# Kernel optimization log

Hardware: AMD Instinct MI355X
Metric: run time of the kernel (lower is better)

## Reference

```python
import jax, jax.numpy as jnp
import numpy as np

PARALLISM = 128          # Subarray[0]
O_BITS = 8               # ADC_resolution
SCALE = float(2 ** O_BITS - 1)          # 255.0
MAXCURRENT = 0.02 * PARALLISM           # 2.56 ; a_scale/w_scale == 2**32-1 so guards skip them


def setup_inputs() -> dict:
    key = jax.random.key(0)
    k1, k2, k3 = jax.random.split(key, 3)
    B, K, N = 8192, 4096, 4096
    x = jax.random.normal(k1, (B, K), dtype=jnp.float32) * 0.1
    weight = jax.random.normal(k2, (N, K), dtype=jnp.float32)  # torch Linear layout [out, in]
    bias = jax.random.normal(k3, (N,), dtype=jnp.float32)
    return {"x": x, "weight": weight, "bias": bias, "layer": 1}


def _quantize_partial(x):
    # output_quantize.forward: clamp to +/-maxcurrent, scale to [−scale, scale], round (STE), rescale
    y = jnp.clip(x, -MAXCURRENT, MAXCURRENT)
    y = y / MAXCURRENT * SCALE
    y = y + jax.lax.stop_gradient(jnp.round(y) - y)  # Round.apply with straight-through grad
    return y / SCALE * MAXCURRENT


def reference(x, weight, bias, layer):
    # Hard_fc: chunked VMM along the input-feature (row) dim with per-subarray ADC quantization
    B, K = x.shape
    w = weight.T                      # [K, N]
    N = w.shape[1]
    num = K // PARALLISM              # K chosen divisible by PARALLISM (32 chunks)
    xc = x.reshape(B, num, PARALLISM).swapaxes(0, 1)       # [num, B, P]
    wc = w.reshape(num, PARALLISM, N)                       # [num, P, N]

    def step(acc, chunk):
        xi, wi = chunk                # [B, P], [P, N]
        return acc + _quantize_partial(xi @ wi), None

    acc0 = jnp.zeros((B, N), dtype=x.dtype)
    out, _ = jax.lax.scan(step, acc0, (xc, wc))
    out = out + bias
    return out.reshape(B, -1)
```

## Files before the change

### kernel.cpp

```cpp
#include <hip/hip_runtime.h>


typedef __attribute__((ext_vector_type(8))) short short8;
typedef __attribute__((ext_vector_type(4))) float floatx4;

#define BM 128
#define BN 128
#define BK 64

static __device__ __forceinline__ unsigned short f2bf(float f) {
    union { float f; unsigned int u; } v; v.f = f;
    unsigned int u = v.u;
    unsigned int r = (u + 0x7fffu + ((u >> 16) & 1u)) >> 16;
    return (unsigned short)r;
}

__global__ void cast_x_kernel(const float* __restrict__ in,
                              unsigned short* __restrict__ out, int n4) {
    int i = blockIdx.x * 256 + threadIdx.x;
    if (i >= n4) return;
    float4 v = ((const float4*)in)[i];
    ushort4 o;
    o.x = f2bf(v.x); o.y = f2bf(v.y); o.z = f2bf(v.z); o.w = f2bf(v.w);
    ((ushort4*)out)[i] = o;
}

__global__ void cast_w_kernel(const float* __restrict__ in,
                              unsigned short* __restrict__ out, int n4) {
    const float s = 99.609375f;
    int i = blockIdx.x * 256 + threadIdx.x;
    if (i >= n4) return;
    float4 v = ((const float4*)in)[i];
    ushort4 o;
    o.x = f2bf(v.x * s); o.y = f2bf(v.y * s); o.z = f2bf(v.z * s); o.w = f2bf(v.w * s);
    ((ushort4*)out)[i] = o;
}

__global__ __launch_bounds__(256, 2) void vmm_kernel(
    const unsigned short* __restrict__ A,
    const unsigned short* __restrict__ Bw,
    const float* __restrict__ bias,
    float* __restrict__ out,
    int N, int K)
{
    __shared__ unsigned short sA[BM * BK];
    __shared__ unsigned short sB[BN * BK];

    const int tid  = threadIdx.x;
    const int wid  = tid >> 6;
    const int lane = tid & 63;

    const int m0 = blockIdx.y * BM;
    const int n0 = blockIdx.x * BN;

    const int waveM = (wid >> 1) * 64;
    const int waveN = (wid & 1) * 64;

    floatx4 acc[4][4];
    floatx4 macc[4][4];
    #pragma unroll
    for (int i = 0; i < 4; ++i)
        #pragma unroll
        for (int j = 0; j < 4; ++j) {
            acc[i][j]  = (floatx4){0.f, 0.f, 0.f, 0.f};
            macc[i][j] = (floatx4){0.f, 0.f, 0.f, 0.f};
        }

    const int srow = lane >> 3;
    const int scol = (lane & 7) * 8;

    const unsigned short* gA = A  + (long)m0 * K;
    const unsigned short* gB = Bw + (long)n0 * K;

    for (int k0 = 0; k0 < K; k0 += BK) {
        #pragma unroll
        for (int i = 0; i < 4; ++i) {
            const int seg = i * 4 + wid;
            const long grow = (long)(seg * 8 + srow);
            __builtin_amdgcn_global_load_lds(
                (const __attribute__((address_space(1))) void*)(gA + grow * K + k0 + scol),
                (__attribute__((address_space(3))) void*)(sA + seg * 512),
                16, 0, 0);
            __builtin_amdgcn_global_load_lds(
                (const __attribute__((address_space(1))) void*)(gB + grow * K + k0 + scol),
                (__attribute__((address_space(3))) void*)(sB + seg * 512),
                16, 0, 0);
        }
        __syncthreads();

        #pragma unroll
        for (int kk = 0; kk < BK; kk += 32) {
            const int krd = kk + (lane >> 4) * 8;
            short8 af[4], bfr[4];
            #pragma unroll
            for (int tm = 0; tm < 4; ++tm)
                af[tm] = *(const short8*)(sA + (waveM + tm * 16 + (lane & 15)) * BK + krd);
            #pragma unroll
            for (int tn = 0; tn < 4; ++tn)
                bfr[tn] = *(const short8*)(sB + (waveN + tn * 16 + (lane & 15)) * BK + krd);
            #pragma unroll
            for (int tm = 0; tm < 4; ++tm)
                #pragma unroll
                for (int tn = 0; tn < 4; ++tn)
                    acc[tm][tn] = __builtin_amdgcn_mfma_f32_16x16x32_bf16(
                        af[tm], bfr[tn], acc[tm][tn], 0, 0, 0);
        }

        if (((k0 + BK) & 127) == 0) {
            #pragma unroll
            for (int tm = 0; tm < 4; ++tm)
                #pragma unroll
                for (int tn = 0; tn < 4; ++tn) {
                    #pragma unroll
                    for (int r = 0; r < 4; ++r) {
                        float v = acc[tm][tn][r];
                        v = __builtin_amdgcn_fmed3f(v, -255.0f, 255.0f);
                        v = __builtin_rintf(v);
                        macc[tm][tn][r] += v;
                    }
                    acc[tm][tn] = (floatx4){0.f, 0.f, 0.f, 0.f};
                }
        }
        __syncthreads();
    }

    const float invs = 2.56f / 255.0f;
    #pragma unroll
    for (int tn = 0; tn < 4; ++tn) {
        const int col = n0 + waveN + tn * 16 + (lane & 15);
        const float bv = bias[col];
        #pragma unroll
        for (int tm = 0; tm < 4; ++tm) {
            const int row = m0 + waveM + tm * 16 + (lane >> 4) * 4;
            #pragma unroll
            for (int r = 0; r < 4; ++r)
                out[(long)(row + r) * N + col] = macc[tm][tn][r] * invs + bv;
        }
    }
}

extern "C" void kernel_launch(void* const* d_in, const int* in_sizes, int n_in,
                              void* d_out, int out_size, void* d_ws, size_t ws_size,
                              hipStream_t stream) {
    const float* x    = (const float*)d_in[0];
    const float* w    = (const float*)d_in[1];
    const float* bias = (const float*)d_in[2];

    const int N = in_sizes[2];
    const int K = in_sizes[1] / N;
    const int B = in_sizes[0] / K;
    float* out = (float*)d_out;

    unsigned short* xb = (unsigned short*)d_ws;
    unsigned short* wb = xb + (size_t)B * K;

    {
        int n4 = (int)(((long)B * K) / 4);
        cast_x_kernel<<<(n4 + 255) / 256, 256, 0, stream>>>(x, xb, n4);
    }
    {
        int n4 = (int)(((long)N * K) / 4);
        cast_w_kernel<<<(n4 + 255) / 256, 256, 0, stream>>>(w, wb, n4);
    }
    dim3 grid(N / BN, B / BM);
    vmm_kernel<<<grid, 256, 0, stream>>>(xb, wb, bias, out, N, K);
}
```

Measured before the change: 725.3 us.

## XOR-swizzle LDS tiles and merge cast kernels into grid-stride 8-wide cast

Applies an XOR swizzle to the 16-byte column chunks when global_load_lds writes A and B tiles to shared memory, and applies the matching swizzle on the MFMA fragment reads. This is meant to remove the LDS bank conflicts that come from 128-byte row strides. The two cast kernels become one grid-stride kernel that converts 8 elements per iteration with a scale parameter, cutting launch size and widening stores. The swizzle must be consistent between write and read or results will be wrong.

```diff
diff --git a/kernel.cpp b/kernel.cpp
--- a/kernel.cpp
+++ b/kernel.cpp
@@ -2,6 +2,7 @@
 
 
 typedef __attribute__((ext_vector_type(8))) short short8;
+typedef __attribute__((ext_vector_type(8))) unsigned short ushort8;
 typedef __attribute__((ext_vector_type(4))) float floatx4;
 
 #define BM 128
@@ -15,25 +16,21 @@
     return (unsigned short)r;
 }
 
-__global__ void cast_x_kernel(const float* __restrict__ in,
-                              unsigned short* __restrict__ out, int n4) {
-    int i = blockIdx.x * 256 + threadIdx.x;
-    if (i >= n4) return;
-    float4 v = ((const float4*)in)[i];
-    ushort4 o;
-    o.x = f2bf(v.x); o.y = f2bf(v.y); o.z = f2bf(v.z); o.w = f2bf(v.w);
-    ((ushort4*)out)[i] = o;
-}
-
-__global__ void cast_w_kernel(const float* __restrict__ in,
-                              unsigned short* __restrict__ out, int n4) {
-    const float s = 99.609375f;
-    int i = blockIdx.x * 256 + threadIdx.x;
-    if (i >= n4) return;
-    float4 v = ((const float4*)in)[i];
-    ushort4 o;
-    o.x = f2bf(v.x * s); o.y = f2bf(v.y * s); o.z = f2bf(v.z * s); o.w = f2bf(v.w * s);
-    ((ushort4*)out)[i] = o;
+__global__ void cast_kernel(const float* __restrict__ in,
+                            unsigned short* __restrict__ out,
+                            long n8, float s) {
+    long i = (long)blockIdx.x * 256 + threadIdx.x;
+    const long stride = (long)gridDim.x * 256;
+    for (; i < n8; i += stride) {
+        float4 a = ((const float4*)in)[2 * i];
+        float4 b = ((const float4*)in)[2 * i + 1];
+        ushort8 o;
+        o[0] = f2bf(a.x * s); o[1] = f2bf(a.y * s);
+        o[2] = f2bf(a.z * s); o[3] = f2bf(a.w * s);
+        o[4] = f2bf(b.x * s); o[5] = f2bf(b.y * s);
+        o[6] = f2bf(b.z * s); o[7] = f2bf(b.w * s);
+        ((ushort8*)out)[i] = o;
+    }
 }
 
 __global__ __launch_bounds__(256, 2) void vmm_kernel(
@@ -67,7 +64,7 @@
         }
 
     const int srow = lane >> 3;
-    const int scol = (lane & 7) * 8;
+    const int scol = (((lane & 7) ^ srow) & 7) * 8;
 
     const unsigned short* gA = A  + (long)m0 * K;
     const unsigned short* gB = Bw + (long)n0 * K;
@@ -90,14 +87,15 @@
 
         #pragma unroll
         for (int kk = 0; kk < BK; kk += 32) {
-            const int krd = kk + (lane >> 4) * 8;
+            const int lc = (kk >> 3) + (lane >> 4);
+            const int pc = (lc ^ (lane & 7)) * 8;
             short8 af[4], bfr[4];
             #pragma unroll
             for (int tm = 0; tm < 4; ++tm)
-                af[tm] = *(const short8*)(sA + (waveM + tm * 16 + (lane & 15)) * BK + krd);
+                af[tm] = *(const short8*)(sA + (waveM + tm * 16 + (lane & 15)) * BK + pc);
             #pragma unroll
             for (int tn = 0; tn < 4; ++tn)
-                bfr[tn] = *(const short8*)(sB + (waveN + tn * 16 + (lane & 15)) * BK + krd);
+                bfr[tn] = *(const short8*)(sB + (waveN + tn * 16 + (lane & 15)) * BK + pc);
             #pragma unroll
             for (int tm = 0; tm < 4; ++tm)
                 #pragma unroll
@@ -154,14 +152,9 @@
     unsigned short* xb = (unsigned short*)d_ws;
     unsigned short* wb = xb + (size_t)B * K;
 
-    {
-        int n4 = (int)(((long)B * K) / 4);
-        cast_x_kernel<<<(n4 + 255) / 256, 256, 0, stream>>>(x, xb, n4);
-    }
-    {
-        int n4 = (int)(((long)N * K) / 4);
-        cast_w_kernel<<<(n4 + 255) / 256, 256, 0, stream>>>(w, wb, n4);
-    }
+    cast_kernel<<<2048, 256, 0, stream>>>(x, xb, ((long)B * K) / 8, 1.0f);
+    cast_kernel<<<2048, 256, 0, stream>>>(w, wb, ((long)N * K) / 8, 99.609375f);
+
     dim3 grid(N / BN, B / BM);
     vmm_kernel<<<grid, 256, 0, stream>>>(xb, wb, bias, out, N, K);
 }
```

After: 650.5 us. 1.11x faster.
